# Kernel tuning notes

Measured on AMD Instinct MI355X. Metric: run time of the kernel, lower is better.

The kernel has to match this reference:

```python
import jax, jax.numpy as jnp
import numpy as np

B, S, D, H = 4, 2048, 1024, 16
DK = D // H
NEG = -1e9


def setup_inputs() -> dict:
    key = jax.random.key(0)
    ks = jax.random.split(key, 11)
    s = 1.0 / np.sqrt(D)
    inp = {
        "query": jax.random.normal(ks[0], (B, S, D), jnp.float32),
        "key": jax.random.normal(ks[1], (B, S, D), jnp.float32),
        "value": jax.random.normal(ks[2], (B, S, D), jnp.float32),
        # causal mask, broadcastable to [B, H, S, S]; 0 -> masked
        "mask": jnp.tril(jnp.ones((S, S), dtype=bool))[None, None],
        # torch Linear weights: [out, in], y = x @ W.T + b
        "Wq": jax.random.uniform(ks[3], (D, D), jnp.float32, -s, s),
        "bq": jax.random.uniform(ks[4], (D,), jnp.float32, -s, s),
        "Wk": jax.random.uniform(ks[5], (D, D), jnp.float32, -s, s),
        "bk": jax.random.uniform(ks[6], (D,), jnp.float32, -s, s),
        "Wv": jax.random.uniform(ks[7], (D, D), jnp.float32, -s, s),
        "bv": jax.random.uniform(ks[8], (D,), jnp.float32, -s, s),
        "Wo": jax.random.uniform(ks[9], (D, D), jnp.float32, -s, s),
        "bo": jax.random.uniform(ks[10], (D,), jnp.float32, -s, s),
    }
    return inp


def reference(query, key, value, mask, Wq, bq, Wk, bk, Wv, bv, Wo, bo):
    def proj(x, W, b):
        y = jnp.einsum('bsd,ed->bse', x, W) + b          # torch Linear: x @ W.T + b
        return y.reshape(B, S, H, DK).transpose(0, 2, 1, 3)  # [B, H, S, DK]

    Q = proj(query, Wq, bq)
    K = proj(key, Wk, bk)
    V = proj(value, Wv, bv)

    scale = 1.0 / np.sqrt(DK)
    scores = jnp.einsum('bhqd,bhkd->bhqk', Q, K) * scale  # [B, H, S, S]
    scores = jnp.where(mask, scores, NEG)
    attn = jax.nn.softmax(scores, axis=-1)
    out = jnp.einsum('bhqk,bhkd->bhqd', attn, V)          # [B, H, S, DK]
    out = out.transpose(0, 2, 1, 3).reshape(B, S, D)
    return jnp.einsum('bsd,ed->bse', out, Wo) + bo
```

## Files before the change

kernel.cpp:

```cpp
#include <hip/hip_runtime.h>
#include <stdint.h>

typedef __attribute__((ext_vector_type(8))) short bf16x8;
typedef __attribute__((ext_vector_type(4))) short s16x4;
typedef __attribute__((ext_vector_type(4))) float f32x4;
typedef __attribute__((ext_vector_type(16))) float f32x16;
typedef __attribute__((ext_vector_type(2))) unsigned u32x2;

#define DEVI __device__ __forceinline__

constexpr int B_ = 4, S_ = 2048, D_ = 1024, H_ = 16, DK_ = 64;
constexpr int M_ = B_ * S_;

DEVI short f2bf(float f) {
  union { float f; uint32_t u; } x; x.f = f;
  uint32_t r = x.u + 0x7fffu + ((x.u >> 16) & 1u);
  return (short)(uint16_t)(r >> 16);
}
DEVI float exp2_hw(float x) {
  float r; asm("v_exp_f32 %0, %1" : "=v"(r) : "v"(x)); return r;
}
DEVI uint32_t cvtpk(float lo, float hi) {
  uint32_t r; asm("v_cvt_pk_bf16_f32 %0, %1, %2" : "=v"(r) : "v"(lo), "v"(hi));
  return r;
}
#if __has_builtin(__builtin_amdgcn_permlane32_swap)
DEVI void plswap(uint32_t& a, uint32_t& b) {
  u32x2 r = __builtin_amdgcn_permlane32_swap(a, b, false, false);
  a = r[0]; b = r[1];
}
#else
DEVI void plswap(uint32_t& a, uint32_t& b) {
  const int h = (threadIdx.x & 63) >> 5;
  const uint32_t pa = (uint32_t)__shfl_xor((int)a, 32);
  const uint32_t pb = (uint32_t)__shfl_xor((int)b, 32);
  const uint32_t na = h ? pb : a;
  const uint32_t nb = h ? b : pa;
  a = na; b = nb;
}
#endif
DEVI void gload16(const short* g, short* l) {
  __builtin_amdgcn_global_load_lds((const __attribute__((address_space(1))) uint32_t*)g,
                                   (__attribute__((address_space(3))) uint32_t*)l, 16, 0, 0);
}

template <int LOG2G>
__global__ __launch_bounds__(256) void cvt3(const float* __restrict__ s0,
                                            const float* __restrict__ s1,
                                            const float* __restrict__ s2,
                                            const float* __restrict__ s3,
                                            short* __restrict__ d0,
                                            short* __restrict__ d1,
                                            short* __restrict__ d2,
                                            short* __restrict__ d3,
                                            int narr) {
  const int stride = gridDim.x * blockDim.x;
  const int total = narr << LOG2G;
  for (int g = blockIdx.x * blockDim.x + threadIdx.x; g < total; g += stride) {
    const int a = g >> LOG2G;
    const size_t off = (size_t)(g & ((1 << LOG2G) - 1)) * 8;
    const float* src = (a == 0) ? s0 : (a == 1) ? s1 : (a == 2) ? s2 : s3;
    short* dst = (a == 0) ? d0 : (a == 1) ? d1 : (a == 2) ? d2 : d3;
    const f32x4 x = *(const f32x4*)(src + off);
    const f32x4 y = *(const f32x4*)(src + off + 4);
    bf16x8 o;
#pragma unroll
    for (int e = 0; e < 4; ++e) { o[e] = f2bf(x[e]); o[e + 4] = f2bf(y[e]); }
    *(bf16x8*)(dst + off) = o;
  }
}

template <int MODE>
__global__ __launch_bounds__(256) void gemm_bt(const short* __restrict__ A,
                                               const short* __restrict__ Bw,
                                               const float* __restrict__ bias,
                                               void* __restrict__ Cout,
                                               int Kdim, int Ndim, float scale) {
  __shared__ short sA[2][128 * 32];
  __shared__ short sB[2][128 * 32];
  const int tid = threadIdx.x;
  const int wid = tid >> 6, lane = tid & 63;
  const int m0 = blockIdx.x * 128, n0 = blockIdx.y * 128;
  const int wm = wid >> 1, wn = wid & 1;

  f32x4 acc[4][4];
#pragma unroll
  for (int i = 0; i < 4; ++i)
#pragma unroll
    for (int j = 0; j < 4; ++j) acc[i][j] = (f32x4){0.f, 0.f, 0.f, 0.f};

  const int srow = wid * 32 + (lane >> 2);
  const int swzs = (srow & 3) ^ ((srow >> 2) & 3);
  const int scol = ((lane & 3) ^ swzs) * 8;
  const short* gA = A + (size_t)(m0 + srow) * Kdim + scol;
  const short* gB = Bw + (size_t)(n0 + srow) * Kdim + scol;

  auto STAGE = [&](int bi, int kt) {
    short* la = &sA[bi][(wid * 32) * 32];
    short* lb = &sB[bi][(wid * 32) * 32];
    gload16(gA + kt, la);
    gload16(gA + (size_t)16 * Kdim + kt, la + 16 * 32);
    gload16(gB + kt, lb);
    gload16(gB + (size_t)16 * Kdim + kt, lb + 16 * 32);
  };

  STAGE(0, 0);
  __syncthreads();
  int cur = 0;

  const int swzf = (lane & 3) ^ ((lane >> 2) & 3);
  const int cofs = (((lane >> 4) ^ swzf) << 3);

  for (int kt = 0; kt < Kdim; kt += 32) {
    if (kt + 32 < Kdim) STAGE(cur ^ 1, kt + 32);
    bf16x8 af[4], bfr[4];
#pragma unroll
    for (int mf = 0; mf < 4; ++mf)
      af[mf] = *(const bf16x8*)&sA[cur][(wm * 64 + mf * 16 + (lane & 15)) * 32 + cofs];
#pragma unroll
    for (int nf = 0; nf < 4; ++nf)
      bfr[nf] = *(const bf16x8*)&sB[cur][(wn * 64 + nf * 16 + (lane & 15)) * 32 + cofs];
#pragma unroll
    for (int mf = 0; mf < 4; ++mf)
#pragma unroll
      for (int nf = 0; nf < 4; ++nf)
        acc[mf][nf] = __builtin_amdgcn_mfma_f32_16x16x32_bf16(af[mf], bfr[nf], acc[mf][nf], 0, 0, 0);
    __syncthreads();
    cur ^= 1;
  }

#pragma unroll
  for (int mf = 0; mf < 4; ++mf) {
#pragma unroll
    for (int nf = 0; nf < 4; ++nf) {
      const int n = n0 + wn * 64 + nf * 16 + (lane & 15);
      const float bi = bias[n];
      if (MODE == 2) {
        const int m_base = m0 + wm * 64 + mf * 16 + ((lane >> 4) * 4);
        const int b = m_base >> 11, s0 = m_base & 2047;
        s16x4 pk;
#pragma unroll
        for (int r = 0; r < 4; ++r) pk[r] = f2bf(acc[mf][nf][r] + bi);
        *(s16x4*)((short*)Cout + ((size_t)(b * 1024 + n)) * 2048 + s0) = pk;
      } else {
#pragma unroll
        for (int r = 0; r < 4; ++r) {
          const int m = m0 + wm * 64 + mf * 16 + ((lane >> 4) * 4) + r;
          const float vv = (acc[mf][nf][r] + bi) * scale;
          if (MODE == 0)
            ((short*)Cout)[(size_t)m * Ndim + n] = f2bf(vv);
          else
            ((float*)Cout)[(size_t)m * Ndim + n] = vv;
        }
      }
    }
  }
}

__global__ __launch_bounds__(512, 4) void attn_fwd(const short* __restrict__ Qf,
                                                   const short* __restrict__ Kf,
                                                   const short* __restrict__ Vt,
                                                   short* __restrict__ AO) {
  __shared__ short sK[2][64 * 64];
  __shared__ short sV[2][64 * 64];

  const int tid = threadIdx.x, wid = tid >> 6, lane = tid & 63;
  const int h = lane >> 5, ql = lane & 31;
  const int cpx = gridDim.x >> 3;
  const int wg = ((int)blockIdx.x & 7) * cpx + ((int)blockIdx.x >> 3);
  const int bh = wg >> 3;
  const int pi = wg & 7;
  const int b = bh >> 4, hd = bh & 15;
  const int panel = (wid < 4) ? (15 - pi) : pi;
  const int qw = panel * 128 + (wid & 3) * 32;
  const int qg = qw + ql;
  const size_t rowbase = (size_t)b * S_ * D_ + (size_t)hd * DK_;
  const size_t vbase = (size_t)bh * 64 * S_;

  bf16x8 aQ[4];
  {
    const short* qp = Qf + rowbase + (size_t)qg * D_ + h * 8;
#pragma unroll
    for (int d = 0; d < 4; ++d) aQ[d] = *(const bf16x8*)(qp + d * 16);
  }

  f32x16 o0, o1;
#pragma unroll
  for (int i = 0; i < 16; ++i) { o0[i] = 0.f; o1[i] = 0.f; }
  float m_run = -1e30f, lsum = 0.f;

  const int srow8 = lane >> 3;
  const int schunk = ((lane & 7) ^ srow8) * 8;
  const short* gK = Kf + rowbase + (size_t)(wid * 8 + srow8) * D_ + schunk;
  const short* gV = Vt + vbase + (size_t)(wid * 8 + srow8) * S_ + schunk;

  auto STAGE = [&](int bufi, int kt) {
    gload16(gK + (size_t)kt * D_, &sK[bufi][(wid * 8) * 64]);
    gload16(gV + kt, &sV[bufi][(wid * 8) * 64]);
  };

  const int nt = 32 - 2 * pi;
  STAGE(0, 0);
  __syncthreads();
  int cur = 0;

  const int swz = ((ql & 7) << 3);

  for (int t = 0; t < nt; ++t) {
    const int kt = t * 64;
    if (t + 1 < nt) STAGE(cur ^ 1, kt + 64);
    if (kt <= qw + 31) {
      const short* bK = &sK[cur][0];
      const short* bV = &sV[cur][0];
      bf16x8 kf[8];
#pragma unroll
      for (int d = 0; d < 4; ++d) {
        const int co = ((d * 2 + h) << 3) ^ swz;
        kf[d]     = *(const bf16x8*)&bK[ql * 64 + co];
        kf[4 + d] = *(const bf16x8*)&bK[(32 + ql) * 64 + co];
      }
      f32x16 p0, p1;
#pragma unroll
      for (int i = 0; i < 16; ++i) { p0[i] = 0.f; p1[i] = 0.f; }
      __builtin_amdgcn_s_setprio(1);
#pragma unroll
      for (int d = 0; d < 4; ++d) {
        p0 = __builtin_amdgcn_mfma_f32_32x32x16_bf16(kf[d], aQ[d], p0, 0, 0, 0);
        p1 = __builtin_amdgcn_mfma_f32_32x32x16_bf16(kf[4 + d], aQ[d], p1, 0, 0, 0);
      }
      __builtin_amdgcn_s_setprio(0);
      bf16x8 vf[8];
#pragma unroll
      for (int m = 0; m < 4; ++m) {
        const int co = ((m * 2 + h) << 3) ^ swz;
        vf[m]     = *(const bf16x8*)&bV[ql * 64 + co];
        vf[4 + m] = *(const bf16x8*)&bV[(32 + ql) * 64 + co];
      }
      if (kt + 63 > qw) {
        const int qk = qg - kt;
#pragma unroll
        for (int i = 0; i < 16; ++i) {
          const int k0i = 8 * (i >> 2) + 4 * h + (i & 3);
          if (k0i > qk) p0[i] = -1e30f;
          if (k0i + 32 > qk) p1[i] = -1e30f;
        }
      }
      float tr[8];
#pragma unroll
      for (int i = 0; i < 8; ++i)
        tr[i] = fmaxf(fmaxf(p0[i], p0[i + 8]), fmaxf(p1[i], p1[i + 8]));
#pragma unroll
      for (int s = 4; s > 0; s >>= 1)
#pragma unroll
        for (int i = 0; i < s; ++i) tr[i] = fmaxf(tr[i], tr[i + s]);
      float mx = fmaxf(tr[0], __shfl_xor(tr[0], 32));
      if (__any(mx > m_run + 8.f)) {
        const float mnew = fmaxf(m_run, mx);
        const float corr = exp2_hw(m_run - mnew);
        m_run = mnew;
        lsum *= corr;
#pragma unroll
        for (int i = 0; i < 16; ++i) { o0[i] *= corr; o1[i] *= corr; }
      }
#pragma unroll
      for (int i = 0; i < 16; ++i) {
        p0[i] = exp2_hw(p0[i] - m_run);
        p1[i] = exp2_hw(p1[i] - m_run);
      }
      float sr[8];
#pragma unroll
      for (int i = 0; i < 8; ++i) sr[i] = (p0[i] + p0[i + 8]) + (p1[i] + p1[i + 8]);
#pragma unroll
      for (int s = 4; s > 0; s >>= 1)
#pragma unroll
        for (int i = 0; i < s; ++i) sr[i] += sr[i + s];
      lsum += sr[0] + __shfl_xor(sr[0], 32);
      uint32_t cj[8], dj[8];
#pragma unroll
      for (int j = 0; j < 4; ++j) {
        cj[j]     = cvtpk(p0[4 * j], p0[4 * j + 1]);
        dj[j]     = cvtpk(p0[4 * j + 2], p0[4 * j + 3]);
        cj[4 + j] = cvtpk(p1[4 * j], p1[4 * j + 1]);
        dj[4 + j] = cvtpk(p1[4 * j + 2], p1[4 * j + 3]);
      }
      __builtin_amdgcn_s_setprio(1);
#pragma unroll
      for (int m = 0; m < 4; ++m) {
        uint32_t w0 = cj[2 * m], w2 = cj[2 * m + 1];
        plswap(w0, w2);
        uint32_t w1 = dj[2 * m], w3 = dj[2 * m + 1];
        plswap(w1, w3);
        union { uint32_t w[4]; bf16x8 v; } u;
        u.w[0] = w0; u.w[1] = w1; u.w[2] = w2; u.w[3] = w3;
        o0 = __builtin_amdgcn_mfma_f32_32x32x16_bf16(vf[m], u.v, o0, 0, 0, 0);
        o1 = __builtin_amdgcn_mfma_f32_32x32x16_bf16(vf[4 + m], u.v, o1, 0, 0, 0);
      }
      __builtin_amdgcn_s_setprio(0);
    }
    __syncthreads();
    cur ^= 1;
  }

  const float invl = 1.f / lsum;
  short* op = AO + rowbase + (size_t)qg * D_;
#pragma unroll
  for (int j = 0; j < 4; ++j) {
    s16x4 w0, w1;
#pragma unroll
    for (int r = 0; r < 4; ++r) {
      w0[r] = f2bf(o0[4 * j + r] * invl);
      w1[r] = f2bf(o1[4 * j + r] * invl);
    }
    *(s16x4*)(op + 8 * j + 4 * h) = w0;
    *(s16x4*)(op + 32 + 8 * j + 4 * h) = w1;
  }
}

extern "C" void kernel_launch(void* const* d_in, const int* in_sizes, int n_in,
                              void* d_out, int out_size, void* d_ws, size_t ws_size,
                              hipStream_t stream) {
  (void)in_sizes; (void)n_in; (void)out_size; (void)ws_size;
  const float* q  = (const float*)d_in[0];
  const float* k  = (const float*)d_in[1];
  const float* v  = (const float*)d_in[2];
  const float* Wq = (const float*)d_in[4];
  const float* bq = (const float*)d_in[5];
  const float* Wk = (const float*)d_in[6];
  const float* bk = (const float*)d_in[7];
  const float* Wv = (const float*)d_in[8];
  const float* bv = (const float*)d_in[9];
  const float* Wo = (const float*)d_in[10];
  const float* bo = (const float*)d_in[11];

  char* ws = (char*)d_ws;
  const size_t MB = 1ull << 20;
  short* wqb = (short*)(ws + 0 * MB);
  short* wkb = (short*)(ws + 2 * MB);
  short* wvb = (short*)(ws + 4 * MB);
  short* wob = (short*)(ws + 6 * MB);
  short* Qf  = (short*)(ws + 8 * MB);
  short* Kf  = (short*)(ws + 24 * MB);
  short* Vtb = (short*)(ws + 40 * MB);
  short* xq  = (short*)(ws + 56 * MB);
  short* xk  = (short*)(ws + 72 * MB);
  short* xv  = (short*)(ws + 88 * MB);
  short* AO  = xq;

  cvt3<20><<<2048, 256, 0, stream>>>(q, k, v, v, xq, xk, xv, xv, 3);
  cvt3<17><<<1024, 256, 0, stream>>>(Wq, Wk, Wv, Wo, wqb, wkb, wvb, wob, 4);

  dim3 gg(M_ / 128, D_ / 128);
  gemm_bt<0><<<gg, 256, 0, stream>>>(xq, wqb, bq, Qf, D_, D_, 0.125f * 1.4426950408889634f);
  gemm_bt<0><<<gg, 256, 0, stream>>>(xk, wkb, bk, Kf, D_, D_, 1.0f);
  gemm_bt<2><<<gg, 256, 0, stream>>>(xv, wvb, bv, Vtb, D_, D_, 1.0f);

  attn_fwd<<<dim3(512), 512, 0, stream>>>(Qf, Kf, Vtb, AO);

  gemm_bt<1><<<gg, 256, 0, stream>>>(AO, wob, bo, d_out, D_, D_, 1.0f);
}
```

Baseline: 227.3 us.

## Split KV range across two wave groups per block and merge partial softmax

Each block now handles a single 128-row query panel, and its two groups of four waves each process half of the causal KV tiles (split-K within the block), with separate LDS buffers per group. At the end, group 1 writes its running max, sum and output accumulators to LDS and group 0 merges them with rescaling before writing. The grid doubles to 1024 blocks, replacing the old pairing of a long and short panel per block. The change also shortens the max and sum reductions, drops the wave-uniform __any check, and loads K/V fragments just-in-time rather than all up front. The intent is better load balance and more parallelism, at the cost of an extra LDS merge and a barrier.

```diff
diff --git a/kernel.cpp b/kernel.cpp
--- a/kernel.cpp
+++ b/kernel.cpp
@@ -161,21 +161,23 @@
                                                    const short* __restrict__ Kf,
                                                    const short* __restrict__ Vt,
                                                    short* __restrict__ AO) {
-  __shared__ short sK[2][64 * 64];
-  __shared__ short sV[2][64 * 64];
+  __shared__ short sK[2][2][64 * 64];
+  __shared__ short sV[2][2][64 * 64];
 
   const int tid = threadIdx.x, wid = tid >> 6, lane = tid & 63;
   const int h = lane >> 5, ql = lane & 31;
+  const int grp = wid >> 2, ww = wid & 3;
   const int cpx = gridDim.x >> 3;
   const int wg = ((int)blockIdx.x & 7) * cpx + ((int)blockIdx.x >> 3);
-  const int bh = wg >> 3;
-  const int pi = wg & 7;
+  const int bh = wg >> 4;
+  const int panel = 15 - (wg & 15);
   const int b = bh >> 4, hd = bh & 15;
-  const int panel = (wid < 4) ? (15 - pi) : pi;
-  const int qw = panel * 128 + (wid & 3) * 32;
+  const int qw = panel * 128 + ww * 32;
   const int qg = qw + ql;
   const size_t rowbase = (size_t)b * S_ * D_ + (size_t)hd * DK_;
   const size_t vbase = (size_t)bh * 64 * S_;
+  const int ha = panel + 1;
+  const int ktb = grp * ha;
 
   bf16x8 aQ[4];
   {
@@ -191,51 +193,44 @@
 
   const int srow8 = lane >> 3;
   const int schunk = ((lane & 7) ^ srow8) * 8;
-  const short* gK = Kf + rowbase + (size_t)(wid * 8 + srow8) * D_ + schunk;
-  const short* gV = Vt + vbase + (size_t)(wid * 8 + srow8) * S_ + schunk;
-
-  auto STAGE = [&](int bufi, int kt) {
-    gload16(gK + (size_t)kt * D_, &sK[bufi][(wid * 8) * 64]);
-    gload16(gV + kt, &sV[bufi][(wid * 8) * 64]);
+  const short* gK = Kf + rowbase + (size_t)(ww * 16 + srow8) * D_ + schunk;
+  const short* gV = Vt + vbase + (size_t)(ww * 16 + srow8) * S_ + schunk;
+
+  auto STAGE = [&](int bufi, int t) {
+    const int kt = (ktb + t) * 64;
+    short* dk = &sK[bufi][grp][(ww * 16) * 64];
+    short* dv = &sV[bufi][grp][(ww * 16) * 64];
+    gload16(gK + (size_t)kt * D_, dk);
+    gload16(gK + (size_t)(kt + 8) * D_, dk + 8 * 64);
+    gload16(gV + kt, dv);
+    gload16(gV + (size_t)8 * S_ + kt, dv + 8 * 64);
   };
 
-  const int nt = 32 - 2 * pi;
   STAGE(0, 0);
   __syncthreads();
   int cur = 0;
 
   const int swz = ((ql & 7) << 3);
 
-  for (int t = 0; t < nt; ++t) {
-    const int kt = t * 64;
-    if (t + 1 < nt) STAGE(cur ^ 1, kt + 64);
+  for (int t = 0; t < ha; ++t) {
+    const int kt = (ktb + t) * 64;
+    if (t + 1 < ha) STAGE(cur ^ 1, t + 1);
     if (kt <= qw + 31) {
-      const short* bK = &sK[cur][0];
-      const short* bV = &sV[cur][0];
-      bf16x8 kf[8];
+      const short* bK = &sK[cur][grp][0];
+      const short* bV = &sV[cur][grp][0];
+      f32x16 p0, p1;
+#pragma unroll
+      for (int i = 0; i < 16; ++i) { p0[i] = 0.f; p1[i] = 0.f; }
+      __builtin_amdgcn_s_setprio(1);
 #pragma unroll
       for (int d = 0; d < 4; ++d) {
         const int co = ((d * 2 + h) << 3) ^ swz;
-        kf[d]     = *(const bf16x8*)&bK[ql * 64 + co];
-        kf[4 + d] = *(const bf16x8*)&bK[(32 + ql) * 64 + co];
-      }
-      f32x16 p0, p1;
-#pragma unroll
-      for (int i = 0; i < 16; ++i) { p0[i] = 0.f; p1[i] = 0.f; }
-      __builtin_amdgcn_s_setprio(1);
-#pragma unroll
-      for (int d = 0; d < 4; ++d) {
-        p0 = __builtin_amdgcn_mfma_f32_32x32x16_bf16(kf[d], aQ[d], p0, 0, 0, 0);
-        p1 = __builtin_amdgcn_mfma_f32_32x32x16_bf16(kf[4 + d], aQ[d], p1, 0, 0, 0);
+        bf16x8 k0 = *(const bf16x8*)&bK[ql * 64 + co];
+        bf16x8 k1 = *(const bf16x8*)&bK[(32 + ql) * 64 + co];
+        p0 = __builtin_amdgcn_mfma_f32_32x32x16_bf16(k0, aQ[d], p0, 0, 0, 0);
+        p1 = __builtin_amdgcn_mfma_f32_32x32x16_bf16(k1, aQ[d], p1, 0, 0, 0);
       }
       __builtin_amdgcn_s_setprio(0);
-      bf16x8 vf[8];
-#pragma unroll
-      for (int m = 0; m < 4; ++m) {
-        const int co = ((m * 2 + h) << 3) ^ swz;
-        vf[m]     = *(const bf16x8*)&bV[ql * 64 + co];
-        vf[4 + m] = *(const bf16x8*)&bV[(32 + ql) * 64 + co];
-      }
       if (kt + 63 > qw) {
         const int qk = qg - kt;
 #pragma unroll
@@ -245,36 +240,25 @@
           if (k0i + 32 > qk) p1[i] = -1e30f;
         }
       }
-      float tr[8];
-#pragma unroll
-      for (int i = 0; i < 8; ++i)
-        tr[i] = fmaxf(fmaxf(p0[i], p0[i + 8]), fmaxf(p1[i], p1[i + 8]));
-#pragma unroll
-      for (int s = 4; s > 0; s >>= 1)
-#pragma unroll
-        for (int i = 0; i < s; ++i) tr[i] = fmaxf(tr[i], tr[i + s]);
-      float mx = fmaxf(tr[0], __shfl_xor(tr[0], 32));
-      if (__any(mx > m_run + 8.f)) {
-        const float mnew = fmaxf(m_run, mx);
-        const float corr = exp2_hw(m_run - mnew);
-        m_run = mnew;
+      float mx = fmaxf(p0[0], p1[0]);
+#pragma unroll
+      for (int i = 1; i < 16; ++i) mx = fmaxf(mx, fmaxf(p0[i], p1[i]));
+      mx = fmaxf(mx, __shfl_xor(mx, 32));
+      if (mx > m_run + 8.f) {
+        const float corr = exp2_hw(m_run - mx);
+        m_run = mx;
         lsum *= corr;
 #pragma unroll
         for (int i = 0; i < 16; ++i) { o0[i] *= corr; o1[i] *= corr; }
       }
+      float rs = 0.f;
 #pragma unroll
       for (int i = 0; i < 16; ++i) {
-        p0[i] = exp2_hw(p0[i] - m_run);
-        p1[i] = exp2_hw(p1[i] - m_run);
-      }
-      float sr[8];
-#pragma unroll
-      for (int i = 0; i < 8; ++i) sr[i] = (p0[i] + p0[i + 8]) + (p1[i] + p1[i + 8]);
-#pragma unroll
-      for (int s = 4; s > 0; s >>= 1)
-#pragma unroll
-        for (int i = 0; i < s; ++i) sr[i] += sr[i + s];
-      lsum += sr[0] + __shfl_xor(sr[0], 32);
+        p0[i] = exp2_hw(p0[i] - m_run); rs += p0[i];
+        p1[i] = exp2_hw(p1[i] - m_run); rs += p1[i];
+      }
+      rs += __shfl_xor(rs, 32);
+      lsum += rs;
       uint32_t cj[8], dj[8];
 #pragma unroll
       for (int j = 0; j < 4; ++j) {
@@ -292,8 +276,11 @@
         plswap(w1, w3);
         union { uint32_t w[4]; bf16x8 v; } u;
         u.w[0] = w0; u.w[1] = w1; u.w[2] = w2; u.w[3] = w3;
-        o0 = __builtin_amdgcn_mfma_f32_32x32x16_bf16(vf[m], u.v, o0, 0, 0, 0);
-        o1 = __builtin_amdgcn_mfma_f32_32x32x16_bf16(vf[4 + m], u.v, o1, 0, 0, 0);
+        const int co = ((m * 2 + h) << 3) ^ swz;
+        bf16x8 v0 = *(const bf16x8*)&bV[ql * 64 + co];
+        bf16x8 v1 = *(const bf16x8*)&bV[(32 + ql) * 64 + co];
+        o0 = __builtin_amdgcn_mfma_f32_32x32x16_bf16(v0, u.v, o0, 0, 0, 0);
+        o1 = __builtin_amdgcn_mfma_f32_32x32x16_bf16(v1, u.v, o1, 0, 0, 0);
       }
       __builtin_amdgcn_s_setprio(0);
     }
@@ -301,18 +288,39 @@
     cur ^= 1;
   }
 
-  const float invl = 1.f / lsum;
-  short* op = AO + rowbase + (size_t)qg * D_;
-#pragma unroll
-  for (int j = 0; j < 4; ++j) {
-    s16x4 w0, w1;
-#pragma unroll
-    for (int r = 0; r < 4; ++r) {
-      w0[r] = f2bf(o0[4 * j + r] * invl);
-      w1[r] = f2bf(o1[4 * j + r] * invl);
+  float* ml = (float*)&sK[0][0][0];
+  float* ov = (float*)&sV[0][0][0];
+  if (grp == 1) {
+    ml[(ww * 2 + 0) * 64 + lane] = m_run;
+    ml[(ww * 2 + 1) * 64 + lane] = lsum;
+#pragma unroll
+    for (int r = 0; r < 16; ++r) {
+      ov[(ww * 32 + r) * 64 + lane] = o0[r];
+      ov[(ww * 32 + 16 + r) * 64 + lane] = o1[r];
     }
-    *(s16x4*)(op + 8 * j + 4 * h) = w0;
-    *(s16x4*)(op + 32 + 8 * j + 4 * h) = w1;
+  }
+  __syncthreads();
+  if (grp == 0) {
+    const float mb = ml[(ww * 2 + 0) * 64 + lane];
+    const float lb = ml[(ww * 2 + 1) * 64 + lane];
+    const float mm = fmaxf(m_run, mb);
+    const float ca = exp2_hw(m_run - mm);
+    const float cb = exp2_hw(mb - mm);
+    const float invl = 1.f / (lsum * ca + lb * cb);
+    short* op = AO + rowbase + (size_t)qg * D_;
+#pragma unroll
+    for (int j = 0; j < 4; ++j) {
+      s16x4 w0, w1;
+#pragma unroll
+      for (int r = 0; r < 4; ++r) {
+        const float b0 = ov[(ww * 32 + 4 * j + r) * 64 + lane];
+        const float b1 = ov[(ww * 32 + 16 + 4 * j + r) * 64 + lane];
+        w0[r] = f2bf((o0[4 * j + r] * ca + b0 * cb) * invl);
+        w1[r] = f2bf((o1[4 * j + r] * ca + b1 * cb) * invl);
+      }
+      *(s16x4*)(op + 8 * j + 4 * h) = w0;
+      *(s16x4*)(op + 32 + 8 * j + 4 * h) = w1;
+    }
   }
 }
 
@@ -354,7 +362,7 @@
   gemm_bt<0><<<gg, 256, 0, stream>>>(xk, wkb, bk, Kf, D_, D_, 1.0f);
   gemm_bt<2><<<gg, 256, 0, stream>>>(xv, wvb, bv, Vtb, D_, D_, 1.0f);
 
-  attn_fwd<<<dim3(512), 512, 0, stream>>>(Qf, Kf, Vtb, AO);
+  attn_fwd<<<dim3(1024), 512, 0, stream>>>(Qf, Kf, Vtb, AO);
 
   gemm_bt<1><<<gg, 256, 0, stream>>>(AO, wob, bo, d_out, D_, D_, 1.0f);
 }
```

Result: faster. 213.9 us (-5.9%).
